# Performance work log

Hardware: AMD Instinct MI355X
Metric: run time of the kernel (lower is better)

## Reference

```python
import jax, jax.numpy as jnp
import numpy as np

B, T, NT = 2, 2048, 512
DIM, DEPTH, MEL, TDIM = 768, 8, 100, 512
D_INNER, NS, PH, Q = 1536, 128, 64, 64
NH = D_INNER // PH
CONV_DIM = D_INNER + 2 * NS
D_INPROJ = 2 * D_INNER + 2 * NS + NH
KCONV = 4
FFI = 2 * DIM
VOCAB = 257


def _ln(x, eps=1e-6):
    m = jnp.mean(x, -1, keepdims=True)
    v = jnp.mean((x - m) ** 2, -1, keepdims=True)
    return (x - m) * jax.lax.rsqrt(v + eps)


def _mish(x):
    return x * jnp.tanh(jax.nn.softplus(x))


def _dwconv_causal(x, w, b):
    # x: [B,T,C], w: [C,K]  depthwise causal conv (left-pad K-1)
    K = w.shape[1]
    xp = jnp.pad(x, ((0, 0), (K - 1, 0), (0, 0)))
    y = sum(xp[:, k:k + x.shape[1]] * w[:, k] for k in range(K))
    return y + b


def _ssd(xh, Bm, Cm, dt, A):
    # chunked selective-scan (Mamba SSD form). xh [B,T,H,P]; Bm,Cm [B,T,N]; dt [B,T,H]; A [H]
    Bsz, Tt, H, P = xh.shape
    N = Bm.shape[-1]
    Cn = Tt // Q
    xb = (dt[..., None] * xh).reshape(Bsz, Cn, Q, H, P)
    a = (dt * A).reshape(Bsz, Cn, Q, H)
    Bc = Bm.reshape(Bsz, Cn, Q, N)
    Cc = Cm.reshape(Bsz, Cn, Q, N)
    acum = jnp.cumsum(a, axis=2)  # [b,c,q,h]
    # intra-chunk: decay matrix exp(acum_q - acum_s) for s <= q
    Ldec = jnp.exp(acum[:, :, :, None, :] - acum[:, :, None, :, :])  # [b,c,q,s,h]
    mask = jnp.tril(jnp.ones((Q, Q), dtype=bool))
    Ldec = jnp.where(mask[None, None, :, :, None], Ldec, 0.0)
    CB = jnp.einsum('bcqn,bcsn->bcqs', Cc, Bc)
    y_in = jnp.einsum('bcqs,bcqsh,bcshp->bcqhp', CB, Ldec, xb)
    # chunk end-states
    dst = jnp.exp(acum[:, :, -1:, :] - acum)  # [b,c,q,h]
    S = jnp.einsum('bcqh,bcqn,bcqhp->bchpn', dst, Bc, xb)
    atot = jnp.exp(acum[:, :, -1, :])  # [b,c,h] total chunk decay

    def step(Hc, inp):
        at_c, S_c = inp
        return at_c[:, :, None, None] * Hc + S_c, Hc

    H0 = jnp.zeros((Bsz, H, P, N), xh.dtype)
    _, prev = jax.lax.scan(step, H0, (jnp.moveaxis(atot, 1, 0), jnp.moveaxis(S, 1, 0)))
    prev = jnp.moveaxis(prev, 0, 1)  # state entering each chunk [b,c,h,p,n]
    y_out = jnp.einsum('bcqn,bchpn->bcqhp', Cc, prev) * jnp.exp(acum)[..., None]
    return (y_in + y_out).reshape(Bsz, Tt, H, P)


def _forward(x, cond, time, text, text_table, inp_w, inp_b, pos_w1, pos_b1, pos_w2, pos_b2, t_w1, t_b1, t_w2, t_b2, adaln_w, adaln_b, in_w, conv_w, conv_b, dt_bias, A_log, Dp, rms_w, out_w, ff_w1, ff_b1, ff_w2, ff_b2, fin_w, fin_b, proj_w, proj_b):
    # timestep embedding (sinusoidal, scale 1000, freq dim 256 -> MLP)
    half = 128
    freqs = jnp.exp(-jnp.log(10000.0) / (half - 1) * jnp.arange(half, dtype=x.dtype))
    ang = 1000.0 * time[:, None] * freqs[None]
    te = jnp.concatenate([jnp.sin(ang), jnp.cos(ang)], -1)
    tvec = jax.nn.silu(te @ t_w1 + t_b1) @ t_w2 + t_b2  # [B,DIM]
    # text embedding (conv_layers=0 path): shift by 1, pad to seq_len, lookup
    idx = jnp.pad(text + 1, ((0, 0), (0, T - text.shape[1])))
    temb = text_table[idx]  # [B,T,TDIM]
    # input embedding + ConvPositionEmbedding (grouped conv k=31, groups=16, Mish x2)
    h = jnp.concatenate([x, cond, temb], -1) @ inp_w + inp_b  # [B,T,DIM]
    dn = ('NWC', 'WIO', 'NWC')
    p = jax.lax.conv_general_dilated(h, pos_w1, (1,), [(15, 15)], dimension_numbers=dn, feature_group_count=16) + pos_b1
    p = _mish(p)
    p = jax.lax.conv_general_dilated(p, pos_w2, (1,), [(15, 15)], dimension_numbers=dn, feature_group_count=16) + pos_b2
    h = h + _mish(p)
    st = jax.nn.silu(tvec)
    for l in range(DEPTH):
        mod = st @ adaln_w[l] + adaln_b[l]
        sh_msa, sc_msa, g_msa, sh_mlp, sc_mlp, g_mlp = jnp.split(mod, 6, -1)
        xn = _ln(h) * (1 + sc_msa[:, None]) + sh_msa[:, None]
        # Mamba-3 selective scan block
        zxbcdt = xn @ in_w[l]
        z = zxbcdt[..., :D_INNER]
        xBC = zxbcdt[..., D_INNER:D_INNER + CONV_DIM]
        dt = zxbcdt[..., D_INNER + CONV_DIM:]
        xBC = jax.nn.silu(_dwconv_causal(xBC, conv_w[l], conv_b[l]))
        xp = xBC[..., :D_INNER].reshape(B, T, NH, PH)
        Bm = xBC[..., D_INNER:D_INNER + NS]
        Cm = xBC[..., D_INNER + NS:]
        dt = jax.nn.softplus(dt + dt_bias[l])
        A = -jnp.exp(A_log[l])
        y = _ssd(xp, Bm, Cm, dt, A) + Dp[l][:, None] * xp
        y = y.reshape(B, T, D_INNER) * jax.nn.silu(z)
        y = y * jax.lax.rsqrt(jnp.mean(y * y, -1, keepdims=True) + 1e-5) * rms_w[l]
        h = h + g_msa[:, None] * (y @ out_w[l])
        # gated FFN
        xn = _ln(h) * (1 + sc_mlp[:, None]) + sh_mlp[:, None]
        ff = jax.nn.gelu(xn @ ff_w1[l] + ff_b1[l], approximate=True) @ ff_w2[l] + ff_b2[l]
        h = h + g_mlp[:, None] * ff
    fm = st @ fin_w + fin_b
    sc, sh = jnp.split(fm, 2, -1)
    h = _ln(h) * (1 + sc[:, None]) + sh[:, None]
    return h @ proj_w + proj_b


def setup_inputs() -> dict:
    key = jax.random.key(0)
    it = iter(jax.random.split(key, 40))

    def n(shape, s=0.02):
        return (s * jax.random.normal(next(it), shape)).astype(jnp.float32)

    inp = {
        'x': n((B, T, MEL), 1.0),
        'cond': n((B, T, MEL), 1.0),
        'time': jax.random.uniform(next(it), (B,), dtype=jnp.float32),
        'text_table': n((VOCAB, TDIM)),
        'inp_w': n((2 * MEL + TDIM, DIM)), 'inp_b': jnp.zeros((DIM,), jnp.float32),
        'pos_w1': n((31, DIM // 16, DIM), 0.05), 'pos_b1': jnp.zeros((DIM,), jnp.float32),
        'pos_w2': n((31, DIM // 16, DIM), 0.05), 'pos_b2': jnp.zeros((DIM,), jnp.float32),
        't_w1': n((256, DIM)), 't_b1': jnp.zeros((DIM,), jnp.float32),
        't_w2': n((DIM, DIM)), 't_b2': jnp.zeros((DIM,), jnp.float32),
        'adaln_w': n((DEPTH, DIM, 6 * DIM)), 'adaln_b': jnp.zeros((DEPTH, 6 * DIM), jnp.float32),
        'in_w': n((DEPTH, DIM, D_INPROJ)),
        'conv_w': n((DEPTH, CONV_DIM, KCONV), 0.2), 'conv_b': jnp.zeros((DEPTH, CONV_DIM), jnp.float32),
        'dt_bias': n((DEPTH, NH), 0.5),
        'A_log': jnp.log(jnp.tile(jnp.arange(1, NH + 1, dtype=jnp.float32), (DEPTH, 1))),
        'Dp': jnp.ones((DEPTH, NH), jnp.float32),
        'rms_w': jnp.ones((DEPTH, D_INNER), jnp.float32),
        'out_w': n((DEPTH, D_INNER, DIM)),
        'ff_w1': n((DEPTH, DIM, FFI)), 'ff_b1': jnp.zeros((DEPTH, FFI), jnp.float32),
        'ff_w2': n((DEPTH, FFI, DIM)), 'ff_b2': jnp.zeros((DEPTH, DIM), jnp.float32),
        'fin_w': n((DIM, 2 * DIM)), 'fin_b': jnp.zeros((2 * DIM,), jnp.float32),
        'proj_w': n((DIM, MEL)), 'proj_b': jnp.zeros((MEL,), jnp.float32),
    }
    inp['text'] = jax.random.randint(next(it), (B, NT), 0, 256)
    return inp


def reference(x, cond, time, text, text_table, inp_w, inp_b, pos_w1, pos_b1, pos_w2, pos_b2, t_w1, t_b1, t_w2, t_b2, adaln_w, adaln_b, in_w, conv_w, conv_b, dt_bias, A_log, Dp, rms_w, out_w, ff_w1, ff_b1, ff_w2, ff_b2, fin_w, fin_b, proj_w, proj_b):
    return _forward(x, cond, time, text, text_table, inp_w, inp_b, pos_w1, pos_b1, pos_w2, pos_b2, t_w1, t_b1, t_w2, t_b2, adaln_w, adaln_b, in_w, conv_w, conv_b, dt_bias, A_log, Dp, rms_w, out_w, ff_w1, ff_b1, ff_w2, ff_b2, fin_w, fin_b, proj_w, proj_b)
```

## Files before the change

### kernel.cpp

```cpp
#include <hip/hip_runtime.h>
#include <math.h>

constexpr int Bv = 2, Tv = 2048, NTv = 512;
constexpr int DIMv = 768, DEPTHv = 8, MELv = 100, TDIMv = 512;
constexpr int DINNER = 1536, NSv = 128, PHv = 64, QQv = 64;
constexpr int NHv = DINNER / PHv;
constexpr int CONVD = DINNER + 2 * NSv;
constexpr int DINP = 2 * DINNER + 2 * NSv + NHv;
constexpr int KCONVv = 4, FFIv = 2 * DIMv;
constexpr int CNv = Tv / QQv;
constexpr int PCK = 1504;
constexpr int KCAT = 736;

typedef unsigned short u16;
typedef unsigned int u32;
typedef __attribute__((ext_vector_type(8))) short short8v;
typedef __attribute__((ext_vector_type(4))) float f32x4;

__device__ __forceinline__ float siluf(float x) { return x / (1.f + expf(-x)); }
__device__ __forceinline__ float softplusf(float x) { return x > 20.f ? x : log1pf(expf(x)); }
__device__ __forceinline__ float mishf(float x) { return x * tanhf(softplusf(x)); }

__device__ __forceinline__ u16 f2bf(float v) {
    u32 u = __builtin_bit_cast(u32, v);
    u32 r = (u + 0x7fffu + ((u >> 16) & 1u)) >> 16;
    return (u16)r;
}
__device__ __forceinline__ float bf2f(u16 v) {
    u32 u = (u32)v << 16;
    return __builtin_bit_cast(float, u);
}

__device__ __forceinline__ void gload16(const void* g, void* l) {
    __builtin_amdgcn_global_load_lds(
        (const __attribute__((address_space(1))) u32*)g,
        (__attribute__((address_space(3))) u32*)l, 16, 0, 0);
}

__device__ __forceinline__ float blockReduceSum(float v) {
    __shared__ float red[4];
    #pragma unroll
    for (int off = 32; off > 0; off >>= 1) v += __shfl_down(v, off, 64);
    __syncthreads();
    if ((threadIdx.x & 63) == 0) red[threadIdx.x >> 6] = v;
    __syncthreads();
    return red[0] + red[1] + red[2] + red[3];
}

template <int EPI>
__global__ __launch_bounds__(256) void gemm_bf16(const u16* __restrict__ A,
        const u16* __restrict__ BT, const float* __restrict__ bias,
        float* __restrict__ Cf, u16* __restrict__ Cb,
        int M, int N, int K, int ldc,
        const float* __restrict__ modv, int goff, int mstride) {
    __shared__ __align__(16) u16 As[2][64 * 32];
    __shared__ __align__(16) u16 Bs[2][128 * 32];
    const int tid = threadIdx.x;
    const int m0 = blockIdx.y * 64, n0 = blockIdx.x * 128;
    const int lane = tid & 63;
    const int wid = tid >> 6;
    const int wn = wid * 32;
    f32x4 acc[4][2] = {};
    const int srow = tid >> 2, sseg = (tid & 3) * 8;
    const u16* Ag = A + (size_t)(m0 + srow) * K + sseg;
    const u16* Bg = BT + (size_t)(n0 + srow) * K + sseg;
    const int lr = lane & 15, lk = (lane >> 4) * 8;
    gload16(Ag, &As[0][tid * 8]);
    gload16(Bg, &Bs[0][tid * 8]);
    gload16(Bg + (size_t)64 * K, &Bs[0][tid * 8 + 64 * 32]);
    __syncthreads();
    int cur = 0;
    for (int k0 = 0; k0 < K; k0 += 32) {
        if (k0 + 32 < K) {
            const int nb = cur ^ 1, kn = k0 + 32;
            gload16(Ag + kn, &As[nb][tid * 8]);
            gload16(Bg + kn, &Bs[nb][tid * 8]);
            gload16(Bg + kn + (size_t)64 * K, &Bs[nb][tid * 8 + 64 * 32]);
        }
        short8v a_f[4], b_f[2];
        #pragma unroll
        for (int i = 0; i < 4; i++)
            a_f[i] = *(const short8v*)&As[cur][(i * 16 + lr) * 32 + lk];
        #pragma unroll
        for (int j = 0; j < 2; j++)
            b_f[j] = *(const short8v*)&Bs[cur][(wn + j * 16 + lr) * 32 + lk];
        #pragma unroll
        for (int i = 0; i < 4; i++)
            #pragma unroll
            for (int j = 0; j < 2; j++)
                acc[i][j] = __builtin_amdgcn_mfma_f32_16x16x32_bf16(a_f[i], b_f[j], acc[i][j], 0, 0, 0);
        __syncthreads();
        cur ^= 1;
    }
    const int r0 = (lane >> 4) * 4;
    #pragma unroll
    for (int i = 0; i < 4; i++) {
        #pragma unroll
        for (int j = 0; j < 2; j++) {
            const int col = n0 + wn + j * 16 + lr;
            if (col >= N) continue;
            const int row = m0 + i * 16 + r0;
            const float bv = (EPI == 1 || EPI == 2 || EPI == 4) ? bias[col] : 0.f;
            #pragma unroll
            for (int r = 0; r < 4; r++) {
                float v = acc[i][j][r] + bv;
                if (EPI == 2) {
                    float xx = v;
                    v = 0.5f * xx * (1.f + tanhf(0.7978845608028654f * (xx + 0.044715f * xx * xx * xx)));
                    Cb[(size_t)(row + r) * ldc + col] = f2bf(v);
                } else if (EPI == 3 || EPI == 4) {
                    const int bb = (row + r) >> 11;
                    float g = modv[(size_t)bb * mstride + goff + col];
                    Cf[(size_t)(row + r) * ldc + col] += g * v;
                } else {
                    Cf[(size_t)(row + r) * ldc + col] = v;
                }
            }
        }
    }
}

__global__ __launch_bounds__(256) void wt_convert(const float* __restrict__ W,
        u16* __restrict__ WT, int K, int N, int Kmax) {
    __shared__ float t[32][33];
    const int n0 = blockIdx.x * 32, k0 = blockIdx.y * 32;
    const int c = threadIdx.x & 31, rq = (threadIdx.x >> 5) * 4;
    #pragma unroll
    for (int i = 0; i < 4; i++) {
        int n = n0 + c, k = k0 + rq + i;
        t[rq + i][c] = (n < N && k < Kmax) ? W[(size_t)k * N + n] : 0.f;
    }
    __syncthreads();
    #pragma unroll
    for (int i = 0; i < 4; i++)
        WT[(size_t)(n0 + rq + i) * K + k0 + c] = f2bf(t[c][rq + i]);
}

__global__ __launch_bounds__(256) void pw_convert(const float* __restrict__ w,
        u16* __restrict__ WT) {
    __shared__ float t[32][33];
    const int kk0 = blockIdx.x * 32, o0 = blockIdx.y * 32;
    const int c = threadIdx.x & 31, rq = (threadIdx.x >> 5) * 4;
    #pragma unroll
    for (int i = 0; i < 4; i++) {
        int kk = kk0 + rq + i;
        t[rq + i][c] = (kk < 1488) ? w[(size_t)kk * DIMv + o0 + c] : 0.f;
    }
    __syncthreads();
    #pragma unroll
    for (int i = 0; i < 4; i++)
        WT[(size_t)(o0 + rq + i) * PCK + kk0 + c] = f2bf(t[c][rq + i]);
}

template <int IN_BF, int FUSE>
__global__ __launch_bounds__(256) void posconv_mfma(const void* __restrict__ inv,
        const u16* __restrict__ WT, const float* __restrict__ bias,
        void* __restrict__ outv) {
    __shared__ __align__(16) u16 xs[95 * 48];
    const int t0 = blockIdx.x * 64, g = blockIdx.y, b = blockIdx.z;
    const int tid = threadIdx.x;
    for (int e = tid; e < 95 * 48; e += 256) {
        int rr = e / 48, cc = e % 48;
        int t = t0 - 15 + rr;
        float v = 0.f;
        if (t >= 0 && t < Tv) {
            size_t gi = ((size_t)b * Tv + t) * DIMv + g * 48 + cc;
            v = IN_BF ? bf2f(((const u16*)inv)[gi]) : ((const float*)inv)[gi];
        }
        xs[e] = f2bf(v);
    }
    __syncthreads();
    const int lane = tid & 63, w = tid >> 6;
    const int lr = lane & 15, lq8 = (lane >> 4) * 8, rq = (lane >> 4) * 4;
    const u16* arow = &xs[(w * 16 + lr) * 48 + lq8];
    const u16* brow = &WT[(size_t)(g * 48 + lr) * PCK + lq8];
    f32x4 acc[3] = {};
    #pragma unroll 2
    for (int ks = 0; ks < PCK / 32; ks++) {
        short8v a = *(const short8v*)(arow + ks * 32);
        #pragma unroll
        for (int j = 0; j < 3; j++) {
            short8v bf = *(const short8v*)(brow + (size_t)j * 16 * PCK + ks * 32);
            acc[j] = __builtin_amdgcn_mfma_f32_16x16x32_bf16(a, bf, acc[j], 0, 0, 0);
        }
    }
    #pragma unroll
    for (int j = 0; j < 3; j++) {
        const int o = g * 48 + j * 16 + lr;
        const float bvv = bias[o];
        #pragma unroll
        for (int r = 0; r < 4; r++) {
            const int t = t0 + w * 16 + rq + r;
            float v = acc[j][r] + bvv;
            size_t gi = ((size_t)b * Tv + t) * DIMv + o;
            if (FUSE == 0) ((u16*)outv)[gi] = f2bf(mishf(v));
            else ((float*)outv)[gi] += mishf(v);
        }
    }
}

__global__ __launch_bounds__(256) void temb1_kernel(const float* __restrict__ timev,
        const float* __restrict__ t_w1, const float* __restrict__ t_b1,
        float* __restrict__ hid) {
    const int b = blockIdx.y;
    const int o = blockIdx.x * 64 + (threadIdx.x & 63);
    const int ks = threadIdx.x >> 6;
    __shared__ float te[256];
    __shared__ float part[4][64];
    {
        int j = threadIdx.x, f = j & 127;
        float fr = expf(-logf(10000.f) / 127.f * (float)f);
        float ang = 1000.f * timev[b] * fr;
        te[j] = (j < 128) ? sinf(ang) : cosf(ang);
    }
    __syncthreads();
    float acc = 0.f;
    #pragma unroll 8
    for (int k = ks * 64; k < ks * 64 + 64; k++) acc += te[k] * t_w1[(size_t)k * DIMv + o];
    part[ks][threadIdx.x & 63] = acc;
    __syncthreads();
    if (threadIdx.x < 64) {
        float r = part[0][threadIdx.x] + part[1][threadIdx.x] + part[2][threadIdx.x] + part[3][threadIdx.x]
                + t_b1[o];
        hid[b * DIMv + o] = siluf(r);
    }
}

__global__ __launch_bounds__(256) void temb2_kernel(const float* __restrict__ hid,
        const float* __restrict__ t_w2, const float* __restrict__ t_b2,
        float* __restrict__ st_out) {
    const int b = blockIdx.y;
    const int o = blockIdx.x * 64 + (threadIdx.x & 63);
    const int ks = threadIdx.x >> 6;
    __shared__ float hv[DIMv];
    __shared__ float part[4][64];
    for (int j = threadIdx.x; j < DIMv; j += 256) hv[j] = hid[b * DIMv + j];
    __syncthreads();
    float acc = 0.f;
    #pragma unroll 8
    for (int k = ks * 192; k < ks * 192 + 192; k++) acc += hv[k] * t_w2[(size_t)k * DIMv + o];
    part[ks][threadIdx.x & 63] = acc;
    __syncthreads();
    if (threadIdx.x < 64) {
        float r = part[0][threadIdx.x] + part[1][threadIdx.x] + part[2][threadIdx.x] + part[3][threadIdx.x]
                + t_b2[o];
        st_out[b * DIMv + o] = siluf(r);
    }
}

__global__ __launch_bounds__(256) void modvec_kernel(const float* __restrict__ st,
        const float* __restrict__ W, const float* __restrict__ bias,
        float* __restrict__ out, int N) {
    const int l = blockIdx.z, b = blockIdx.y;
    const int o = blockIdx.x * 64 + (threadIdx.x & 63);
    const int ks = threadIdx.x >> 6;
    __shared__ float sv[DIMv];
    __shared__ float part[4][64];
    for (int j = threadIdx.x; j < DIMv; j += 256) sv[j] = st[b * DIMv + j];
    __syncthreads();
    const float* Wl = W + (size_t)l * DIMv * N + o;
    float acc = 0.f;
    #pragma unroll 8
    for (int k = ks * 192; k < ks * 192 + 192; k++) acc += sv[k] * Wl[(size_t)k * N];
    part[ks][threadIdx.x & 63] = acc;
    __syncthreads();
    if (threadIdx.x < 64) {
        float r = part[0][threadIdx.x] + part[1][threadIdx.x] + part[2][threadIdx.x] + part[3][threadIdx.x]
                + bias[(size_t)l * N + o];
        out[((size_t)l * Bv + b) * N + o] = r;
    }
}

__global__ void concat_bf16(const float* __restrict__ x, const float* __restrict__ cond,
                            const float* __restrict__ table, const int* __restrict__ text,
                            u16* __restrict__ cat) {
    size_t i = (size_t)blockIdx.x * 256 + threadIdx.x;
    const size_t total = (size_t)Bv * Tv * KCAT;
    if (i >= total) return;
    int j = (int)(i % KCAT);
    size_t row = i / KCAT;
    int t = (int)(row % Tv), b = (int)(row / Tv);
    float v = 0.f;
    if (j < MELv) v = x[row * MELv + j];
    else if (j < 2 * MELv) v = cond[row * MELv + (j - MELv)];
    else if (j < 712) {
        int idx = (t < NTv) ? (text[b * NTv + t] + 1) : 0;
        v = table[(size_t)idx * TDIMv + (j - 2 * MELv)];
    }
    cat[i] = f2bf(v);
}

template <int BF>
__global__ __launch_bounds__(256) void ln_mod_kernel(const float* __restrict__ h,
        void* __restrict__ outv, const float* __restrict__ modv,
        int sc_off, int sh_off, int mod_stride) {
    const int row = blockIdx.x;
    const int b = row / Tv;
    const float* hr = h + (size_t)row * DIMv;
    float s = 0.f;
    for (int j = threadIdx.x; j < DIMv; j += 256) s += hr[j];
    s = blockReduceSum(s);
    const float m = s / DIMv;
    float v = 0.f;
    for (int j = threadIdx.x; j < DIMv; j += 256) { float d = hr[j] - m; v += d * d; }
    v = blockReduceSum(v);
    const float rstd = rsqrtf(v / DIMv + 1e-6f);
    const float* mb = modv + (size_t)b * mod_stride;
    for (int j = threadIdx.x; j < DIMv; j += 256) {
        float val = (hr[j] - m) * rstd * (1.f + mb[sc_off + j]) + mb[sh_off + j];
        if (BF) ((u16*)outv)[(size_t)row * DIMv + j] = f2bf(val);
        else ((float*)outv)[(size_t)row * DIMv + j] = val;
    }
}

__global__ void dwconv_kernel(const float* __restrict__ zx, const float* __restrict__ cw,
                              const float* __restrict__ cb, float* __restrict__ xbc) {
    size_t i = (size_t)blockIdx.x * 256 + threadIdx.x;
    if (i >= (size_t)Bv * Tv * CONVD) return;
    int c = (int)(i % CONVD);
    size_t row = i / CONVD;
    int t = (int)(row % Tv);
    const float* base = zx + row * DINP + DINNER + c;
    float acc = cb[c];
    #pragma unroll
    for (int k = 0; k < KCONVv; k++) {
        int d = k - 3;
        if (t + d >= 0) acc += base[(ptrdiff_t)d * DINP] * cw[c * KCONVv + k];
    }
    xbc[i] = siluf(acc);
}

__global__ __launch_bounds__(256) void ssd_cb(const float* __restrict__ xbc,
                                              float* __restrict__ CBg) {
    constexpr int ST = 136;
    __shared__ __align__(16) u16 Cs[64 * ST];
    __shared__ __align__(16) u16 Bs[64 * ST];
    const int c = blockIdx.x, b = blockIdx.y;
    const int tid = threadIdx.x;
    const size_t rowbase = (size_t)b * Tv + (size_t)c * QQv;
    for (int e = tid; e < 64 * 128; e += 256) {
        int r = e >> 7, n = e & 127;
        const float* src = &xbc[(rowbase + r) * CONVD + DINNER];
        Bs[r * ST + n] = f2bf(src[n]);
        Cs[r * ST + n] = f2bf(src[NSv + n]);
    }
    __syncthreads();
    const int lane = tid & 63, w = tid >> 6;
    const int lr = lane & 15, lk8 = (lane >> 4) * 8, rq = (lane >> 4) * 4;
    f32x4 acc[4] = {};
    #pragma unroll
    for (int ks = 0; ks < 4; ks++) {
        short8v a = *(const short8v*)&Cs[(w * 16 + lr) * ST + ks * 32 + lk8];
        #pragma unroll
        for (int j = 0; j < 4; j++) {
            short8v bf = *(const short8v*)&Bs[(j * 16 + lr) * ST + ks * 32 + lk8];
            acc[j] = __builtin_amdgcn_mfma_f32_16x16x32_bf16(a, bf, acc[j], 0, 0, 0);
        }
    }
    float* out = CBg + ((size_t)(b * CNv + c)) * 4096;
    #pragma unroll
    for (int j = 0; j < 4; j++)
        #pragma unroll
        for (int r = 0; r < 4; r++)
            out[(w * 16 + rq + r) * 64 + j * 16 + lr] = acc[j][r];
}

__global__ __launch_bounds__(256) void ssd_part1m(const float* __restrict__ xbc,
        const float* __restrict__ zx, const float* __restrict__ dt_bias,
        const float* __restrict__ A_log,
        const float* __restrict__ CBg, float* __restrict__ ybuf,
        float* __restrict__ Sg, float* __restrict__ acg, float* __restrict__ atg) {
    constexpr int ST64 = 72;
    __shared__ __align__(16) u16 xbT[64 * ST64];
    __shared__ __align__(16) u16 Wsm[64 * ST64];
    __shared__ __align__(16) u16 BT[128 * ST64];
    __shared__ float ac[64], dts[64], erev[64];
    const int h = blockIdx.x, c = blockIdx.y, b = blockIdx.z;
    const int tid = threadIdx.x;
    const size_t rowbase = (size_t)b * Tv + (size_t)c * QQv;
    const size_t bch = ((size_t)b * CNv + c) * NHv + h;
    if (tid < 64) {
        float raw = zx[(rowbase + tid) * DINP + DINNER + CONVD + h] + dt_bias[h];
        float dtv = softplusf(raw);
        dts[tid] = dtv;
        float v = dtv * (-expf(A_log[h]));
        #pragma unroll
        for (int off = 1; off < 64; off <<= 1) {
            float t = __shfl_up(v, off, 64);
            if (tid >= off) v += t;
        }
        ac[tid] = v;
    }
    __syncthreads();
    const float ac63 = ac[63];
    if (tid < 64) {
        erev[tid] = expf(ac63 - ac[tid]);
        acg[bch * 64 + tid] = ac[tid];
        if (tid == 63) atg[bch] = expf(ac63);
    }
    for (int e = tid; e < 64 * 64; e += 256) {
        int s = e >> 6, p = e & 63;
        xbT[p * ST64 + s] = f2bf(dts[s] * xbc[(rowbase + s) * CONVD + h * PHv + p]);
    }
    for (int e = tid; e < 64 * 128; e += 256) {
        int s = e >> 7, n = e & 127;
        BT[n * ST64 + s] = f2bf(xbc[(rowbase + s) * CONVD + DINNER + n]);
    }
    {
        const float* cbrow = CBg + ((size_t)(b * CNv + c)) * 4096;
        for (int e = tid; e < 64 * 64; e += 256) {
            int q = e >> 6, s = e & 63;
            float wv = (s <= q) ? cbrow[e] * expf(ac[q] - ac[s]) : 0.f;
            Wsm[q * ST64 + s] = f2bf(wv);
        }
    }
    __syncthreads();
    const int lane = tid & 63, w = tid >> 6;
    const int lr = lane & 15, lk8 = (lane >> 4) * 8, rq = (lane >> 4) * 4;
    {
        f32x4 acc[4] = {};
        #pragma unroll
        for (int ks = 0; ks < 2; ks++) {
            short8v bf = *(const short8v*)&xbT[(w * 16 + lr) * ST64 + ks * 32 + lk8];
            #pragma unroll
            for (int i = 0; i < 4; i++) {
                short8v a = *(const short8v*)&Wsm[(i * 16 + lr) * ST64 + ks * 32 + lk8];
                acc[i] = __builtin_amdgcn_mfma_f32_16x16x32_bf16(a, bf, acc[i], 0, 0, 0);
            }
        }
        #pragma unroll
        for (int i = 0; i < 4; i++)
            #pragma unroll
            for (int r = 0; r < 4; r++) {
                int q = i * 16 + rq + r, p = w * 16 + lr;
                ybuf[(rowbase + q) * DINNER + h * PHv + p] = acc[i][r];
            }
    }
    __syncthreads();
    for (int e = tid; e < 64 * 64; e += 256) {
        int p = e >> 6, s = e & 63;
        xbT[p * ST64 + s] = f2bf(bf2f(xbT[p * ST64 + s]) * erev[s]);
    }
    __syncthreads();
    {
        f32x4 acc[4][2] = {};
        #pragma unroll
        for (int ks = 0; ks < 2; ks++) {
            short8v a[4];
            #pragma unroll
            for (int i = 0; i < 4; i++)
                a[i] = *(const short8v*)&xbT[(i * 16 + lr) * ST64 + ks * 32 + lk8];
            #pragma unroll
            for (int j = 0; j < 2; j++) {
                short8v bf = *(const short8v*)&BT[(w * 32 + j * 16 + lr) * ST64 + ks * 32 + lk8];
                #pragma unroll
                for (int i = 0; i < 4; i++)
                    acc[i][j] = __builtin_amdgcn_mfma_f32_16x16x32_bf16(a[i], bf, acc[i][j], 0, 0, 0);
            }
        }
        float* So = Sg + bch * (PHv * NSv);
        #pragma unroll
        for (int i = 0; i < 4; i++)
            #pragma unroll
            for (int j = 0; j < 2; j++)
                #pragma unroll
                for (int r = 0; r < 4; r++)
                    So[(i * 16 + rq + r) * NSv + w * 32 + j * 16 + lr] = acc[i][j][r];
    }
}

__global__ void ssd_scan(float* __restrict__ Sg, const float* __restrict__ atg) {
    int idx = blockIdx.x * 256 + threadIdx.x;
    if (idx >= Bv * NHv * PHv * NSv) return;
    int n = idx % NSv;
    int p = (idx / NSv) % PHv;
    int h = (idx / (NSv * PHv)) % NHv;
    int b = idx / (NSv * PHv * NHv);
    float H = 0.f;
    for (int c = 0; c < CNv; c++) {
        size_t bch = ((size_t)b * CNv + c) * NHv + h;
        size_t off = bch * PHv * NSv + (size_t)p * NSv + n;
        float s = Sg[off];
        float at = atg[bch];
        Sg[off] = H;
        H = at * H + s;
    }
}

__global__ __launch_bounds__(256) void ssd_part2m(const float* __restrict__ xbc,
        const float* __restrict__ Sg, const float* __restrict__ acg,
        const float* __restrict__ Dp, float* __restrict__ ybuf) {
    constexpr int ST = 136;
    __shared__ __align__(16) u16 Cs[64 * ST];
    __shared__ __align__(16) u16 Ps[64 * ST];
    __shared__ float eac[64];
    const int h = blockIdx.x, c = blockIdx.y, b = blockIdx.z;
    const int tid = threadIdx.x;
    const size_t rowbase = (size_t)b * Tv + (size_t)c * QQv;
    const size_t bch = ((size_t)b * CNv + c) * NHv + h;
    if (tid < 64) eac[tid] = expf(acg[bch * 64 + tid]);
    for (int e = tid; e < 64 * 128; e += 256) {
        int r = e >> 7, n = e & 127;
        Cs[r * ST + n] = f2bf(xbc[(rowbase + r) * CONVD + DINNER + NSv + n]);
        Ps[r * ST + n] = f2bf(Sg[bch * (PHv * NSv) + e]);
    }
    __syncthreads();
    const int lane = tid & 63, w = tid >> 6;
    const int lr = lane & 15, lk8 = (lane >> 4) * 8, rq = (lane >> 4) * 4;
    f32x4 acc[4] = {};
    #pragma unroll
    for (int ks = 0; ks < 4; ks++) {
        short8v bf = *(const short8v*)&Ps[(w * 16 + lr) * ST + ks * 32 + lk8];
        #pragma unroll
        for (int i = 0; i < 4; i++) {
            short8v a = *(const short8v*)&Cs[(i * 16 + lr) * ST + ks * 32 + lk8];
            acc[i] = __builtin_amdgcn_mfma_f32_16x16x32_bf16(a, bf, acc[i], 0, 0, 0);
        }
    }
    const float Dh = Dp[h];
    #pragma unroll
    for (int i = 0; i < 4; i++)
        #pragma unroll
        for (int r = 0; r < 4; r++) {
            int q = i * 16 + rq + r, p = w * 16 + lr;
            size_t row = rowbase + q;
            size_t yi = row * DINNER + h * PHv + p;
            float xv = xbc[row * CONVD + h * PHv + p];
            ybuf[yi] += acc[i][r] * eac[q] + Dh * xv;
        }
}

__global__ __launch_bounds__(256) void gate_rms_kernel(const float* __restrict__ y,
        const float* __restrict__ zx, const float* __restrict__ rms_w,
        u16* __restrict__ yb) {
    const int row = blockIdx.x;
    const float* yr = y + (size_t)row * DINNER;
    const float* zr = zx + (size_t)row * DINP;
    float local[6];
    float ss = 0.f;
    #pragma unroll
    for (int i = 0; i < 6; i++) {
        int j = threadIdx.x + i * 256;
        float v = yr[j] * siluf(zr[j]);
        local[i] = v;
        ss += v * v;
    }
    ss = blockReduceSum(ss);
    const float scale = rsqrtf(ss / DINNER + 1e-5f);
    #pragma unroll
    for (int i = 0; i < 6; i++) {
        int j = threadIdx.x + i * 256;
        yb[(size_t)row * DINNER + j] = f2bf(local[i] * scale * rms_w[j]);
    }
}

extern "C" void kernel_launch(void* const* d_in, const int* in_sizes, int n_in,
                              void* d_out, int out_size, void* d_ws, size_t ws_size,
                              hipStream_t stream) {
    int s3 = (in_sizes[3] == Bv * NTv) ? 1 : 0;
    const float* x      = (const float*)d_in[0];
    const float* cond   = (const float*)d_in[1];
    const float* timev  = (const float*)d_in[2];
    const int*   text   = (const int*)(s3 ? d_in[3] : d_in[32]);
    const float* table  = (const float*)d_in[3 + s3];
    const float* inp_w  = (const float*)d_in[4 + s3];
    const float* inp_b  = (const float*)d_in[5 + s3];
    const float* pos_w1 = (const float*)d_in[6 + s3];
    const float* pos_b1 = (const float*)d_in[7 + s3];
    const float* pos_w2 = (const float*)d_in[8 + s3];
    const float* pos_b2 = (const float*)d_in[9 + s3];
    const float* t_w1   = (const float*)d_in[10 + s3];
    const float* t_b1   = (const float*)d_in[11 + s3];
    const float* t_w2   = (const float*)d_in[12 + s3];
    const float* t_b2   = (const float*)d_in[13 + s3];
    const float* adaln_w= (const float*)d_in[14 + s3];
    const float* adaln_b= (const float*)d_in[15 + s3];
    const float* in_w   = (const float*)d_in[16 + s3];
    const float* conv_w = (const float*)d_in[17 + s3];
    const float* conv_b = (const float*)d_in[18 + s3];
    const float* dt_bias= (const float*)d_in[19 + s3];
    const float* A_log  = (const float*)d_in[20 + s3];
    const float* Dp     = (const float*)d_in[21 + s3];
    const float* rms_w  = (const float*)d_in[22 + s3];
    const float* out_w  = (const float*)d_in[23 + s3];
    const float* ff_w1  = (const float*)d_in[24 + s3];
    const float* ff_b1  = (const float*)d_in[25 + s3];
    const float* ff_w2  = (const float*)d_in[26 + s3];
    const float* ff_b2  = (const float*)d_in[27 + s3];
    const float* fin_w  = (const float*)d_in[28 + s3];
    const float* fin_b  = (const float*)d_in[29 + s3];
    const float* proj_w = (const float*)d_in[30 + s3];
    const float* proj_b = (const float*)d_in[31 + s3];

    float* ws = (float*)d_ws;
    const size_t n_h = (size_t)Bv * Tv * DIMv;
    size_t off = 0;
    auto nx = [&](size_t n) { float* p = ws + off; off += n; return p; };
    float* h_   = nx(n_h);
    float* zx_  = nx((size_t)Bv * Tv * DINP);
    float* xbc_ = nx((size_t)Bv * Tv * CONVD);
    float* y_   = nx((size_t)Bv * Tv * DINNER);
    float* S_   = nx((size_t)Bv * CNv * NHv * PHv * NSv);
    float* ac_  = nx((size_t)Bv * CNv * NHv * QQv);
    float* at_  = nx((size_t)Bv * CNv * NHv);
    float* CB_  = nx((size_t)Bv * CNv * QQv * QQv);
    float* st_  = nx((size_t)Bv * DIMv);
    float* hid_ = nx((size_t)Bv * DIMv);
    float* mod_ = nx((size_t)DEPTHv * Bv * 6 * DIMv);
    float* fm_  = nx((size_t)Bv * 2 * DIMv);
    off = (off + 15) & ~(size_t)15;
    u16* wt_   = (u16*)(ws + off);
    u16* xnb_  = wt_  + (size_t)3456 * 768;
    u16* actb_ = xnb_ + (size_t)4096 * 768;
    u16* xnb2_ = actb_ + (size_t)4096 * 1536;
    u16* pwt_  = xnb2_ + (size_t)4096 * 768;
    u16* catb_ = pwt_ + (size_t)768 * PCK;

    const int MT = Bv * Tv;

    temb1_kernel<<<dim3(DIMv / 64, Bv), 256, 0, stream>>>(timev, t_w1, t_b1, hid_);
    temb2_kernel<<<dim3(DIMv / 64, Bv), 256, 0, stream>>>(hid_, t_w2, t_b2, st_);
    modvec_kernel<<<dim3(6 * DIMv / 64, Bv, DEPTHv), 256, 0, stream>>>(st_, adaln_w, adaln_b, mod_, 6 * DIMv);
    modvec_kernel<<<dim3(2 * DIMv / 64, Bv, 1), 256, 0, stream>>>(st_, fin_w, fin_b, fm_, 2 * DIMv);

    concat_bf16<<<(unsigned)(((size_t)Bv * Tv * KCAT + 255) / 256), 256, 0, stream>>>(
        x, cond, table, text, catb_);
    wt_convert<<<dim3(768 / 32, KCAT / 32), 256, 0, stream>>>(inp_w, wt_, KCAT, 768, 712);
    gemm_bf16<1><<<dim3(6, 64), 256, 0, stream>>>(
        catb_, wt_, inp_b, h_, nullptr, MT, DIMv, KCAT, DIMv, nullptr, 0, 0);

    pw_convert<<<dim3(PCK / 32, DIMv / 32), 256, 0, stream>>>(pos_w1, pwt_);
    posconv_mfma<0, 0><<<dim3(Tv / 64, 16, Bv), 256, 0, stream>>>(h_, pwt_, pos_b1, xnb2_);
    pw_convert<<<dim3(PCK / 32, DIMv / 32), 256, 0, stream>>>(pos_w2, pwt_);
    posconv_mfma<1, 1><<<dim3(Tv / 64, 16, Bv), 256, 0, stream>>>(xnb2_, pwt_, pos_b2, h_);

    for (int l = 0; l < DEPTHv; l++) {
        const float* modl = mod_ + (size_t)l * Bv * 6 * DIMv;
        ln_mod_kernel<1><<<MT, 256, 0, stream>>>(h_, xnb_, modl, DIMv, 0, 6 * DIMv);
        wt_convert<<<dim3(3456 / 32, 768 / 32), 256, 0, stream>>>(
            in_w + (size_t)l * DIMv * DINP, wt_, DIMv, DINP, DIMv);
        gemm_bf16<0><<<dim3(27, 64), 256, 0, stream>>>(
            xnb_, wt_, nullptr, zx_, nullptr, MT, DINP, DIMv, DINP, nullptr, 0, 0);
        dwconv_kernel<<<(unsigned)(((size_t)Bv * Tv * CONVD + 255) / 256), 256, 0, stream>>>(
            zx_, conv_w + (size_t)l * CONVD * KCONVv, conv_b + (size_t)l * CONVD, xbc_);
        ssd_cb<<<dim3(CNv, Bv), 256, 0, stream>>>(xbc_, CB_);
        ssd_part1m<<<dim3(NHv, CNv, Bv), 256, 0, stream>>>(
            xbc_, zx_, dt_bias + l * NHv, A_log + l * NHv, CB_, y_, S_, ac_, at_);
        ssd_scan<<<(Bv * NHv * PHv * NSv + 255) / 256, 256, 0, stream>>>(S_, at_);
        ssd_part2m<<<dim3(NHv, CNv, Bv), 256, 0, stream>>>(
            xbc_, S_, ac_, Dp + l * NHv, y_);
        gate_rms_kernel<<<MT, 256, 0, stream>>>(y_, zx_, rms_w + (size_t)l * DINNER, actb_);
        wt_convert<<<dim3(768 / 32, 1536 / 32), 256, 0, stream>>>(
            out_w + (size_t)l * DINNER * DIMv, wt_, DINNER, DIMv, DINNER);
        gemm_bf16<3><<<dim3(6, 64), 256, 0, stream>>>(
            actb_, wt_, nullptr, h_, nullptr, MT, DIMv, DINNER, DIMv, modl, 2 * DIMv, 6 * DIMv);
        ln_mod_kernel<1><<<MT, 256, 0, stream>>>(h_, xnb_, modl, 4 * DIMv, 3 * DIMv, 6 * DIMv);
        wt_convert<<<dim3(1536 / 32, 768 / 32), 256, 0, stream>>>(
            ff_w1 + (size_t)l * DIMv * FFIv, wt_, DIMv, FFIv, DIMv);
        gemm_bf16<2><<<dim3(12, 64), 256, 0, stream>>>(
            xnb_, wt_, ff_b1 + (size_t)l * FFIv, nullptr, actb_, MT, FFIv, DIMv, FFIv, nullptr, 0, 0);
        wt_convert<<<dim3(768 / 32, 1536 / 32), 256, 0, stream>>>(
            ff_w2 + (size_t)l * FFIv * DIMv, wt_, FFIv, DIMv, FFIv);
        gemm_bf16<4><<<dim3(6, 64), 256, 0, stream>>>(
            actb_, wt_, ff_b2 + (size_t)l * DIMv, h_, nullptr, MT, DIMv, FFIv, DIMv, modl, 5 * DIMv, 6 * DIMv);
    }

    ln_mod_kernel<1><<<MT, 256, 0, stream>>>(h_, xnb_, fm_, 0, DIMv, 2 * DIMv);
    wt_convert<<<dim3(128 / 32, 768 / 32), 256, 0, stream>>>(proj_w, wt_, DIMv, MELv, DIMv);
    gemm_bf16<1><<<dim3(1, 64), 256, 0, stream>>>(
        xnb_, wt_, proj_b, (float*)d_out, nullptr, MT, MELv, DIMv, MELv, nullptr, 0, 0);
}
```

Measured before the change: 2.830 ms.

## Store Mamba intermediates in bf16 and add 128x128 GEMM tile variant

```diff
diff --git a/kernel.cpp b/kernel.cpp
--- a/kernel.cpp
+++ b/kernel.cpp
@@ -30,6 +30,7 @@
     u32 u = (u32)v << 16;
     return __builtin_bit_cast(float, u);
 }
+__device__ __forceinline__ float bf2fs(short v) { return bf2f((u16)v); }
 
 __device__ __forceinline__ void gload16(const void* g, void* l) {
     __builtin_amdgcn_global_load_lds(
@@ -47,25 +48,30 @@
     return red[0] + red[1] + red[2] + red[3];
 }
 
-template <int EPI>
+template <int EPI, int BIG>
 __global__ __launch_bounds__(256) void gemm_bf16(const u16* __restrict__ A,
         const u16* __restrict__ BT, const float* __restrict__ bias,
         float* __restrict__ Cf, u16* __restrict__ Cb,
         int M, int N, int K, int ldc,
         const float* __restrict__ modv, int goff, int mstride) {
-    __shared__ __align__(16) u16 As[2][64 * 32];
+    constexpr int BM = BIG ? 128 : 64;
+    constexpr int MI = BIG ? 4 : 4;
+    constexpr int NJ = BIG ? 4 : 2;
+    __shared__ __align__(16) u16 As[2][BM * 32];
     __shared__ __align__(16) u16 Bs[2][128 * 32];
     const int tid = threadIdx.x;
-    const int m0 = blockIdx.y * 64, n0 = blockIdx.x * 128;
+    const int m0 = blockIdx.y * BM, n0 = blockIdx.x * 128;
     const int lane = tid & 63;
     const int wid = tid >> 6;
-    const int wn = wid * 32;
-    f32x4 acc[4][2] = {};
+    const int wm = BIG ? (wid >> 1) * 64 : 0;
+    const int wn = BIG ? (wid & 1) * 64 : wid * 32;
+    f32x4 acc[MI][NJ] = {};
     const int srow = tid >> 2, sseg = (tid & 3) * 8;
     const u16* Ag = A + (size_t)(m0 + srow) * K + sseg;
     const u16* Bg = BT + (size_t)(n0 + srow) * K + sseg;
     const int lr = lane & 15, lk = (lane >> 4) * 8;
     gload16(Ag, &As[0][tid * 8]);
+    if (BIG) gload16(Ag + (size_t)64 * K, &As[0][tid * 8 + 64 * 32]);
     gload16(Bg, &Bs[0][tid * 8]);
     gload16(Bg + (size_t)64 * K, &Bs[0][tid * 8 + 64 * 32]);
     __syncthreads();
@@ -74,37 +80,40 @@
         if (k0 + 32 < K) {
             const int nb = cur ^ 1, kn = k0 + 32;
             gload16(Ag + kn, &As[nb][tid * 8]);
+            if (BIG) gload16(Ag + kn + (size_t)64 * K, &As[nb][tid * 8 + 64 * 32]);
             gload16(Bg + kn, &Bs[nb][tid * 8]);
             gload16(Bg + kn + (size_t)64 * K, &Bs[nb][tid * 8 + 64 * 32]);
         }
-        short8v a_f[4], b_f[2];
-        #pragma unroll
-        for (int i = 0; i < 4; i++)
-            a_f[i] = *(const short8v*)&As[cur][(i * 16 + lr) * 32 + lk];
-        #pragma unroll
-        for (int j = 0; j < 2; j++)
+        short8v a_f[MI], b_f[NJ];
+        #pragma unroll
+        for (int i = 0; i < MI; i++)
+            a_f[i] = *(const short8v*)&As[cur][(wm + i * 16 + lr) * 32 + lk];
+        #pragma unroll
+        for (int j = 0; j < NJ; j++)
             b_f[j] = *(const short8v*)&Bs[cur][(wn + j * 16 + lr) * 32 + lk];
         #pragma unroll
-        for (int i = 0; i < 4; i++)
+        for (int i = 0; i < MI; i++)
             #pragma unroll
-            for (int j = 0; j < 2; j++)
+            for (int j = 0; j < NJ; j++)
                 acc[i][j] = __builtin_amdgcn_mfma_f32_16x16x32_bf16(a_f[i], b_f[j], acc[i][j], 0, 0, 0);
         __syncthreads();
         cur ^= 1;
     }
     const int r0 = (lane >> 4) * 4;
     #pragma unroll
-    for (int i = 0; i < 4; i++) {
-        #pragma unroll
-        for (int j = 0; j < 2; j++) {
+    for (int i = 0; i < MI; i++) {
+        #pragma unroll
+        for (int j = 0; j < NJ; j++) {
             const int col = n0 + wn + j * 16 + lr;
             if (col >= N) continue;
-            const int row = m0 + i * 16 + r0;
+            const int row = m0 + wm + i * 16 + r0;
             const float bv = (EPI == 1 || EPI == 2 || EPI == 4) ? bias[col] : 0.f;
             #pragma unroll
             for (int r = 0; r < 4; r++) {
                 float v = acc[i][j][r] + bv;
-                if (EPI == 2) {
+                if (EPI == 0) {
+                    Cb[(size_t)(row + r) * ldc + col] = f2bf(v);
+                } else if (EPI == 2) {
                     float xx = v;
                     v = 0.5f * xx * (1.f + tanhf(0.7978845608028654f * (xx + 0.044715f * xx * xx * xx)));
                     Cb[(size_t)(row + r) * ldc + col] = f2bf(v);
@@ -313,24 +322,34 @@
     }
 }
 
-__global__ void dwconv_kernel(const float* __restrict__ zx, const float* __restrict__ cw,
-                              const float* __restrict__ cb, float* __restrict__ xbc) {
+__global__ void dwconv_kernel(const u16* __restrict__ zxb, const float* __restrict__ cw,
+                              const float* __restrict__ cb, u16* __restrict__ xbcb) {
     size_t i = (size_t)blockIdx.x * 256 + threadIdx.x;
-    if (i >= (size_t)Bv * Tv * CONVD) return;
-    int c = (int)(i % CONVD);
-    size_t row = i / CONVD;
-    int t = (int)(row % Tv);
-    const float* base = zx + row * DINP + DINNER + c;
-    float acc = cb[c];
+    const size_t total = (size_t)Bv * Tv * (CONVD / 8);
+    if (i >= total) return;
+    const int c8 = (int)(i % (CONVD / 8)) * 8;
+    const size_t row = i / (CONVD / 8);
+    const int t = (int)(row % Tv);
+    const u16* base = zxb + row * DINP + DINNER + c8;
+    float acc[8];
+    #pragma unroll
+    for (int u = 0; u < 8; u++) acc[u] = cb[c8 + u];
     #pragma unroll
     for (int k = 0; k < KCONVv; k++) {
-        int d = k - 3;
-        if (t + d >= 0) acc += base[(ptrdiff_t)d * DINP] * cw[c * KCONVv + k];
-    }
-    xbc[i] = siluf(acc);
-}
-
-__global__ __launch_bounds__(256) void ssd_cb(const float* __restrict__ xbc,
+        const int d = k - 3;
+        if (t + d < 0) continue;
+        short8v tv = *(const short8v*)(base + (ptrdiff_t)d * DINP);
+        #pragma unroll
+        for (int u = 0; u < 8; u++)
+            acc[u] += bf2fs(tv[u]) * cw[(c8 + u) * KCONVv + k];
+    }
+    short8v outv;
+    #pragma unroll
+    for (int u = 0; u < 8; u++) outv[u] = (short)f2bf(siluf(acc[u]));
+    *(short8v*)(xbcb + row * CONVD + c8) = outv;
+}
+
+__global__ __launch_bounds__(256) void ssd_cb(const u16* __restrict__ xbcb,
                                               float* __restrict__ CBg) {
     constexpr int ST = 136;
     __shared__ __align__(16) u16 Cs[64 * ST];
@@ -338,11 +357,11 @@
     const int c = blockIdx.x, b = blockIdx.y;
     const int tid = threadIdx.x;
     const size_t rowbase = (size_t)b * Tv + (size_t)c * QQv;
-    for (int e = tid; e < 64 * 128; e += 256) {
-        int r = e >> 7, n = e & 127;
-        const float* src = &xbc[(rowbase + r) * CONVD + DINNER];
-        Bs[r * ST + n] = f2bf(src[n]);
-        Cs[r * ST + n] = f2bf(src[NSv + n]);
+    for (int e = tid; e < 64 * 16; e += 256) {
+        int r = e >> 4, n8 = (e & 15) * 8;
+        const u16* src = &xbcb[(rowbase + r) * CONVD + DINNER];
+        *(short8v*)&Bs[r * ST + n8] = *(const short8v*)(src + n8);
+        *(short8v*)&Cs[r * ST + n8] = *(const short8v*)(src + NSv + n8);
     }
     __syncthreads();
     const int lane = tid & 63, w = tid >> 6;
@@ -365,10 +384,10 @@
             out[(w * 16 + rq + r) * 64 + j * 16 + lr] = acc[j][r];
 }
 
-__global__ __launch_bounds__(256) void ssd_part1m(const float* __restrict__ xbc,
-        const float* __restrict__ zx, const float* __restrict__ dt_bias,
+__global__ __launch_bounds__(256) void ssd_part1m(const u16* __restrict__ xbcb,
+        const u16* __restrict__ zxb, const float* __restrict__ dt_bias,
         const float* __restrict__ A_log,
-        const float* __restrict__ CBg, float* __restrict__ ybuf,
+        const float* __restrict__ CBg, u16* __restrict__ ybuf,
         float* __restrict__ Sg, float* __restrict__ acg, float* __restrict__ atg) {
     constexpr int ST64 = 72;
     __shared__ __align__(16) u16 xbT[64 * ST64];
@@ -380,7 +399,7 @@
     const size_t rowbase = (size_t)b * Tv + (size_t)c * QQv;
     const size_t bch = ((size_t)b * CNv + c) * NHv + h;
     if (tid < 64) {
-        float raw = zx[(rowbase + tid) * DINP + DINNER + CONVD + h] + dt_bias[h];
+        float raw = bf2f(zxb[(rowbase + tid) * DINP + DINNER + CONVD + h]) + dt_bias[h];
         float dtv = softplusf(raw);
         dts[tid] = dtv;
         float v = dtv * (-expf(A_log[h]));
@@ -400,11 +419,11 @@
     }
     for (int e = tid; e < 64 * 64; e += 256) {
         int s = e >> 6, p = e & 63;
-        xbT[p * ST64 + s] = f2bf(dts[s] * xbc[(rowbase + s) * CONVD + h * PHv + p]);
+        xbT[p * ST64 + s] = f2bf(dts[s] * bf2f(xbcb[(rowbase + s) * CONVD + h * PHv + p]));
     }
     for (int e = tid; e < 64 * 128; e += 256) {
         int s = e >> 7, n = e & 127;
-        BT[n * ST64 + s] = f2bf(xbc[(rowbase + s) * CONVD + DINNER + n]);
+        BT[n * ST64 + s] = xbcb[(rowbase + s) * CONVD + DINNER + n];
     }
     {
         const float* cbrow = CBg + ((size_t)(b * CNv + c)) * 4096;
@@ -433,7 +452,7 @@
             #pragma unroll
             for (int r = 0; r < 4; r++) {
                 int q = i * 16 + rq + r, p = w * 16 + lr;
-                ybuf[(rowbase + q) * DINNER + h * PHv + p] = acc[i][r];
+                ybuf[(rowbase + q) * DINNER + h * PHv + p] = f2bf(acc[i][r]);
             }
     }
     __syncthreads();
@@ -487,9 +506,9 @@
     }
 }
 
-__global__ __launch_bounds__(256) void ssd_part2m(const float* __restrict__ xbc,
+__global__ __launch_bounds__(256) void ssd_part2m(const u16* __restrict__ xbcb,
         const float* __restrict__ Sg, const float* __restrict__ acg,
-        const float* __restrict__ Dp, float* __restrict__ ybuf) {
+        const float* __restrict__ Dp, u16* __restrict__ ybuf) {
     constexpr int ST = 136;
     __shared__ __align__(16) u16 Cs[64 * ST];
     __shared__ __align__(16) u16 Ps[64 * ST];
@@ -499,10 +518,16 @@
     const size_t rowbase = (size_t)b * Tv + (size_t)c * QQv;
     const size_t bch = ((size_t)b * CNv + c) * NHv + h;
     if (tid < 64) eac[tid] = expf(acg[bch * 64 + tid]);
-    for (int e = tid; e < 64 * 128; e += 256) {
-        int r = e >> 7, n = e & 127;
-        Cs[r * ST + n] = f2bf(xbc[(rowbase + r) * CONVD + DINNER + NSv + n]);
-        Ps[r * ST + n] = f2bf(Sg[bch * (PHv * NSv) + e]);
+    for (int e = tid; e < 64 * 16; e += 256) {
+        int r = e >> 4, n8 = (e & 15) * 8;
+        *(short8v*)&Cs[r * ST + n8] =
+            *(const short8v*)&xbcb[(rowbase + r) * CONVD + DINNER + NSv + n8];
+    }
+    for (int e = tid; e < 64 * 32; e += 256) {
+        int r = e >> 5, n4 = (e & 31) * 4;
+        f32x4 pv = *(const f32x4*)&Sg[bch * (PHv * NSv) + (size_t)r * NSv + n4];
+        u16* dst = &Ps[r * ST + n4];
+        dst[0] = f2bf(pv[0]); dst[1] = f2bf(pv[1]); dst[2] = f2bf(pv[2]); dst[3] = f2bf(pv[3]);
     }
     __syncthreads();
     const int lane = tid & 63, w = tid >> 6;
@@ -525,32 +550,38 @@
             int q = i * 16 + rq + r, p = w * 16 + lr;
             size_t row = rowbase + q;
             size_t yi = row * DINNER + h * PHv + p;
-            float xv = xbc[row * CONVD + h * PHv + p];
-            ybuf[yi] += acc[i][r] * eac[q] + Dh * xv;
-        }
-}
-
-__global__ __launch_bounds__(256) void gate_rms_kernel(const float* __restrict__ y,
-        const float* __restrict__ zx, const float* __restrict__ rms_w,
+            float xv = bf2f(xbcb[row * CONVD + h * PHv + p]);
+            ybuf[yi] = f2bf(bf2f(ybuf[yi]) + acc[i][r] * eac[q] + Dh * xv);
+        }
+}
+
+__global__ __launch_bounds__(256) void gate_rms_kernel(const u16* __restrict__ y,
+        const u16* __restrict__ zxb, const float* __restrict__ rms_w,
         u16* __restrict__ yb) {
     const int row = blockIdx.x;
-    const float* yr = y + (size_t)row * DINNER;
-    const float* zr = zx + (size_t)row * DINP;
-    float local[6];
+    const u16* yr = y + (size_t)row * DINNER;
+    const u16* zr = zxb + (size_t)row * DINP;
+    float vals[8];
     float ss = 0.f;
-    #pragma unroll
-    for (int i = 0; i < 6; i++) {
-        int j = threadIdx.x + i * 256;
-        float v = yr[j] * siluf(zr[j]);
-        local[i] = v;
-        ss += v * v;
+    const int tid = threadIdx.x;
+    if (tid < 192) {
+        short8v yv = *(const short8v*)(yr + tid * 8);
+        short8v zv = *(const short8v*)(zr + tid * 8);
+        #pragma unroll
+        for (int u = 0; u < 8; u++) {
+            float v = bf2fs(yv[u]) * siluf(bf2fs(zv[u]));
+            vals[u] = v;
+            ss += v * v;
+        }
     }
     ss = blockReduceSum(ss);
     const float scale = rsqrtf(ss / DINNER + 1e-5f);
-    #pragma unroll
-    for (int i = 0; i < 6; i++) {
-        int j = threadIdx.x + i * 256;
-        yb[(size_t)row * DINNER + j] = f2bf(local[i] * scale * rms_w[j]);
+    if (tid < 192) {
+        short8v outv;
+        #pragma unroll
+        for (int u = 0; u < 8; u++)
+            outv[u] = (short)f2bf(vals[u] * scale * rms_w[tid * 8 + u]);
+        *(short8v*)(yb + (size_t)row * DINNER + tid * 8) = outv;
     }
 }
 
@@ -597,9 +628,6 @@
     size_t off = 0;
     auto nx = [&](size_t n) { float* p = ws + off; off += n; return p; };
     float* h_   = nx(n_h);
-    float* zx_  = nx((size_t)Bv * Tv * DINP);
-    float* xbc_ = nx((size_t)Bv * Tv * CONVD);
-    float* y_   = nx((size_t)Bv * Tv * DINNER);
     float* S_   = nx((size_t)Bv * CNv * NHv * PHv * NSv);
     float* ac_  = nx((size_t)Bv * CNv * NHv * QQv);
     float* at_  = nx((size_t)Bv * CNv * NHv);
@@ -610,11 +638,14 @@
     float* fm_  = nx((size_t)Bv * 2 * DIMv);
     off = (off + 15) & ~(size_t)15;
     u16* wt_   = (u16*)(ws + off);
-    u16* xnb_  = wt_  + (size_t)3456 * 768;
-    u16* actb_ = xnb_ + (size_t)4096 * 768;
+    u16* zxb_  = wt_   + (size_t)3456 * 768;
+    u16* xbcb_ = zxb_  + (size_t)4096 * DINP;
+    u16* yb_   = xbcb_ + (size_t)4096 * CONVD;
+    u16* xnb_  = yb_   + (size_t)4096 * 1536;
+    u16* actb_ = xnb_  + (size_t)4096 * 768;
     u16* xnb2_ = actb_ + (size_t)4096 * 1536;
     u16* pwt_  = xnb2_ + (size_t)4096 * 768;
-    u16* catb_ = pwt_ + (size_t)768 * PCK;
+    u16* catb_ = pwt_  + (size_t)768 * PCK;
 
     const int MT = Bv * Tv;
 
@@ -626,7 +657,7 @@
     concat_bf16<<<(unsigned)(((size_t)Bv * Tv * KCAT + 255) / 256), 256, 0, stream>>>(
         x, cond, table, text, catb_);
     wt_convert<<<dim3(768 / 32, KCAT / 32), 256, 0, stream>>>(inp_w, wt_, KCAT, 768, 712);
-    gemm_bf16<1><<<dim3(6, 64), 256, 0, stream>>>(
+    gemm_bf16<1, 0><<<dim3(6, 64), 256, 0, stream>>>(
         catb_, wt_, inp_b, h_, nullptr, MT, DIMv, KCAT, DIMv, nullptr, 0, 0);
 
     pw_convert<<<dim3(PCK / 32, DIMv / 32), 256, 0, stream>>>(pos_w1, pwt_);
@@ -639,34 +670,34 @@
         ln_mod_kernel<1><<<MT, 256, 0, stream>>>(h_, xnb_, modl, DIMv, 0, 6 * DIMv);
         wt_convert<<<dim3(3456 / 32, 768 / 32), 256, 0, stream>>>(
             in_w + (size_t)l * DIMv * DINP, wt_, DIMv, DINP, DIMv);
-        gemm_bf16<0><<<dim3(27, 64), 256, 0, stream>>>(
-            xnb_, wt_, nullptr, zx_, nullptr, MT, DINP, DIMv, DINP, nullptr, 0, 0);
-        dwconv_kernel<<<(unsigned)(((size_t)Bv * Tv * CONVD + 255) / 256), 256, 0, stream>>>(
-            zx_, conv_w + (size_t)l * CONVD * KCONVv, conv_b + (size_t)l * CONVD, xbc_);
-        ssd_cb<<<dim3(CNv, Bv), 256, 0, stream>>>(xbc_, CB_);
+        gemm_bf16<0, 1><<<dim3(27, 32), 256, 0, stream>>>(
+            xnb_, wt_, nullptr, nullptr, zxb_, MT, DINP, DIMv, DINP, nullptr, 0, 0);
+        dwconv_kernel<<<(unsigned)(((size_t)Bv * Tv * (CONVD / 8) + 255) / 256), 256, 0, stream>>>(
+            zxb_, conv_w + (size_t)l * CONVD * KCONVv, conv_b + (size_t)l * CONVD, xbcb_);
+        ssd_cb<<<dim3(CNv, Bv), 256, 0, stream>>>(xbcb_, CB_);
         ssd_part1m<<<dim3(NHv, CNv, Bv), 256, 0, stream>>>(
-            xbc_, zx_, dt_bias + l * NHv, A_log + l * NHv, CB_, y_, S_, ac_, at_);
+            xbcb_, zxb_, dt_bias + l * NHv, A_log + l * NHv, CB_, yb_, S_, ac_, at_);
         ssd_scan<<<(Bv * NHv * PHv * NSv + 255) / 256, 256, 0, stream>>>(S_, at_);
         ssd_part2m<<<dim3(NHv, CNv, Bv), 256, 0, stream>>>(
-            xbc_, S_, ac_, Dp + l * NHv, y_);
-        gate_rms_kernel<<<MT, 256, 0, stream>>>(y_, zx_, rms_w + (size_t)l * DINNER, actb_);
+            xbcb_, S_, ac_, Dp + l * NHv, yb_);
+        gate_rms_kernel<<<MT, 256, 0, stream>>>(yb_, zxb_, rms_w + (size_t)l * DINNER, actb_);
         wt_convert<<<dim3(768 / 32, 1536 / 32), 256, 0, stream>>>(
             out_w + (size_t)l * DINNER * DIMv, wt_, DINNER, DIMv, DINNER);
-        gemm_bf16<3><<<dim3(6, 64), 256, 0, stream>>>(
+        gemm_bf16<3, 0><<<dim3(6, 64), 256, 0, stream>>>(
             actb_, wt_, nullptr, h_, nullptr, MT, DIMv, DINNER, DIMv, modl, 2 * DIMv, 6 * DIMv);
         ln_mod_kernel<1><<<MT, 256, 0, stream>>>(h_, xnb_, modl, 4 * DIMv, 3 * DIMv, 6 * DIMv);
         wt_convert<<<dim3(1536 / 32, 768 / 32), 256, 0, stream>>>(
             ff_w1 + (size_t)l * DIMv * FFIv, wt_, DIMv, FFIv, DIMv);
-        gemm_bf16<2><<<dim3(12, 64), 256, 0, stream>>>(
+        gemm_bf16<2, 1><<<dim3(12, 32), 256, 0, stream>>>(
             xnb_, wt_, ff_b1 + (size_t)l * FFIv, nullptr, actb_, MT, FFIv, DIMv, FFIv, nullptr, 0, 0);
         wt_convert<<<dim3(768 / 32, 1536 / 32), 256, 0, stream>>>(
             ff_w2 + (size_t)l * FFIv * DIMv, wt_, FFIv, DIMv, FFIv);
-        gemm_bf16<4><<<dim3(6, 64), 256, 0, stream>>>(
+        gemm_bf16<4, 0><<<dim3(6, 64), 256, 0, stream>>>(
             actb_, wt_, ff_b2 + (size_t)l * DIMv, h_, nullptr, MT, DIMv, FFIv, DIMv, modl, 5 * DIMv, 6 * DIMv);
     }
 
     ln_mod_kernel<1><<<MT, 256, 0, stream>>>(h_, xnb_, fm_, 0, DIMv, 2 * DIMv);
     wt_convert<<<dim3(128 / 32, 768 / 32), 256, 0, stream>>>(proj_w, wt_, DIMv, MELv, DIMv);
-    gemm_bf16<1><<<dim3(1, 64), 256, 0, stream>>>(
+    gemm_bf16<1, 0><<<dim3(1, 64), 256, 0, stream>>>(
         xnb_, wt_, proj_b, (float*)d_out, nullptr, MT, MELv, DIMv, MELv, nullptr, 0, 0);
 }
```

New measurement: 2.818 ms. No clear change (-0.4%).
